# Kernel tuning notes

Measured on AMD Instinct MI355X. Metric: run time of the kernel, lower is better.

## Reference

```python
import jax, jax.numpy as jnp
import numpy as np
from jax.ops import segment_sum, segment_max

N_NODES = 16384
N_EDGES = 262144
NODE_DIM = 480
HIDDEN = 256
OUT_DIM = 128
HEADS = 4
N_GRAPHS = 256


def setup_inputs() -> dict:
    key = jax.random.key(0)
    ks = jax.random.split(key, 40)
    p = {}
    p['x'] = jax.random.normal(ks[0], (N_NODES, NODE_DIM), jnp.float32)
    p['edge_index'] = jax.random.randint(ks[1], (2, N_EDGES), 0, N_NODES)
    p['edge_attr'] = jax.random.uniform(ks[2], (N_EDGES, 1), dtype=jnp.float32)
    p['batch'] = jnp.sort(jax.random.randint(ks[3], (N_NODES,), 0, N_GRAPHS))
    p['num_graphs'] = N_GRAPHS
    def w(k, shape):
        return jax.random.normal(k, shape, jnp.float32) * 0.05
    i = 4
    for l, (din, h, c) in zip((1, 2, 3), [(NODE_DIM, HEADS, HIDDEN // HEADS), (HIDDEN, HEADS, HIDDEN // HEADS), (HIDDEN, 1, OUT_DIM)]):
        dout = h * c
        p[f'Wl{l}'] = w(ks[i], (din, dout)); i += 1
        p[f'bl{l}'] = jnp.zeros((dout,), jnp.float32)
        p[f'Wr{l}'] = w(ks[i], (din, dout)); i += 1
        p[f'br{l}'] = jnp.zeros((dout,), jnp.float32)
        p[f'We{l}'] = w(ks[i], (1, dout)); i += 1
        p[f'att{l}'] = w(ks[i], (h, c)); i += 1
        p[f'bo{l}'] = jnp.zeros((dout,), jnp.float32)
    for l, d in [(1, HIDDEN), (2, HIDDEN), (3, OUT_DIM)]:
        p[f'g{l}'] = jnp.ones((d,), jnp.float32)
        p[f'b{l}'] = jnp.zeros((d,), jnp.float32)
    p['Wres'] = w(ks[i], (NODE_DIM, HIDDEN))
    return p


def _layer_norm(x, g, b):
    mu = x.mean(-1, keepdims=True)
    v = ((x - mu) ** 2).mean(-1, keepdims=True)
    return (x - mu) * jax.lax.rsqrt(v + 1e-5) * g + b


def _gatv2(x, src, dst, ea, Wl, bl, Wr, br, We, att, bias):
    # PyG GATv2Conv, eval mode (dropout off), add_self_loops=True, fill_value='mean'
    N = x.shape[0]
    H, C = att.shape
    # self-loop edge attr = scatter-mean of incoming edge attrs per node
    deg = segment_sum(jnp.ones((src.shape[0],), x.dtype), dst, num_segments=N)
    loop_ea = segment_sum(ea, dst, num_segments=N) / jnp.maximum(deg, 1.0)[:, None]
    ar = jnp.arange(N, dtype=src.dtype)
    src2 = jnp.concatenate([src, ar])
    dst2 = jnp.concatenate([dst, ar])
    ea2 = jnp.concatenate([ea, loop_ea], axis=0)
    xl = (x @ Wl + bl).reshape(N, H, C)
    xr = (x @ Wr + br).reshape(N, H, C)
    e = (ea2 @ We).reshape(-1, H, C)
    m = jax.nn.leaky_relu(xl[src2] + xr[dst2] + e, 0.2)  # [E', H, C]
    alpha = jnp.einsum('ehc,hc->eh', m, att)
    amax = segment_max(alpha, dst2, num_segments=N)  # [N, H]; every node has a self loop
    ex = jnp.exp(alpha - amax[dst2])
    denom = segment_sum(ex, dst2, num_segments=N)
    a = ex / denom[dst2]
    out = segment_sum(a[:, :, None] * xl[src2], dst2, num_segments=N)  # [N, H, C]
    return out.reshape(N, H * C) + bias


def _forward(x, edge_attr, params, edge_index, batch, num_graphs):
    (Wl1, bl1, Wr1, br1, We1, att1, bo1,
     Wl2, bl2, Wr2, br2, We2, att2, bo2,
     Wl3, bl3, Wr3, br3, We3, att3, bo3,
     g1, b1, g2, b2, g3, b3, Wres) = params
    src, dst = edge_index[0], edge_index[1]
    gelu = lambda t: jax.nn.gelu(t, approximate=False)
    h = gelu(_layer_norm(_gatv2(x, src, dst, edge_attr, Wl1, bl1, Wr1, br1, We1, att1, bo1), g1, b1))
    h = h + x @ Wres
    h2 = gelu(_layer_norm(_gatv2(h, src, dst, edge_attr, Wl2, bl2, Wr2, br2, We2, att2, bo2), g2, b2))
    h2 = h2 + h
    h3 = _layer_norm(_gatv2(h2, src, dst, edge_attr, Wl3, bl3, Wr3, br3, We3, att3, bo3), g3, b3)
    # global mean pool over graphs
    sums = segment_sum(h3, batch, num_segments=num_graphs)
    cnt = segment_sum(jnp.ones((h3.shape[0],), h3.dtype), batch, num_segments=num_graphs)
    return sums / jnp.maximum(cnt, 1.0)[:, None]


def reference(x, edge_index, edge_attr, batch, num_graphs,
              Wl1, bl1, Wr1, br1, We1, att1, bo1,
              Wl2, bl2, Wr2, br2, We2, att2, bo2,
              Wl3, bl3, Wr3, br3, We3, att3, bo3,
              g1, b1, g2, b2, g3, b3, Wres):
    params = (Wl1, bl1, Wr1, br1, We1, att1, bo1,
              Wl2, bl2, Wr2, br2, We2, att2, bo2,
              Wl3, bl3, Wr3, br3, We3, att3, bo3,
              g1, b1, g2, b2, g3, b3, Wres)
    return _forward(x, edge_attr, params, edge_index, batch, num_graphs)
```

## Files before the change

### kernel.cpp

```cpp
#include <hip/hip_runtime.h>
#include <hip/hip_bf16.h>
#include <math.h>

#define NN 16384
#define NE 262144
#define KDIM1 480
#define DHID 256
#define DOUT3 128
#define NG 256

typedef short bf16x8 __attribute__((ext_vector_type(8)));
typedef float f32x4 __attribute__((ext_vector_type(4)));

#define LOG2E 1.44269504088896340736f

__device__ __forceinline__ unsigned short f2bf(float f) {
  unsigned u = __float_as_uint(f);
  unsigned r = (u + 0x7fffu + ((u >> 16) & 1u)) >> 16;
  return (unsigned short)r;
}
__device__ __forceinline__ float bf2f(unsigned short u) {
  return __uint_as_float((unsigned)u << 16);
}

__device__ __forceinline__ void gload_lds16(const void* g, void* l) {
  __builtin_amdgcn_global_load_lds((const __attribute__((address_space(1))) void*)g,
                                   (__attribute__((address_space(3))) void*)l,
                                   16, 0, 0);
}

__device__ __forceinline__ int lower_bound_i(const int* arr, int n, int val) {
  int lo = 0, hi = n;
  while (lo < hi) {
    int mid = (lo + hi) >> 1;
    if (arr[mid] < val) lo = mid + 1; else hi = mid;
  }
  return lo;
}


__global__ __launch_bounds__(256) void k_edge_count(const int* __restrict__ ei,
                                                    const float* __restrict__ ea,
                                                    int* __restrict__ deg,
                                                    float* __restrict__ easum) {
  int e = blockIdx.x * 256 + threadIdx.x;
  if (e >= NE) return;
  int d = ei[NE + e];
  atomicAdd(&deg[d], 1);
  atomicAdd(&easum[d], ea[e]);
}

__global__ __launch_bounds__(1024) void k_scan(const int* __restrict__ deg,
                                               float* __restrict__ easum,
                                               int* __restrict__ offs,
                                               int* __restrict__ cursor,
                                               const int* __restrict__ bat,
                                               float* __restrict__ ginv) {
  __shared__ int sums[1024];
  int t = threadIdx.x;
  int base = t * 16;
  int local[16];
  int s = 0;
#pragma unroll
  for (int i = 0; i < 16; ++i) { local[i] = deg[base + i]; s += local[i]; }
  sums[t] = s;
  __syncthreads();
  for (int d = 1; d < 1024; d <<= 1) {
    int v = (t >= d) ? sums[t - d] : 0;
    __syncthreads();
    sums[t] += v;
    __syncthreads();
  }
  int prefix = (t == 0) ? 0 : sums[t - 1];
#pragma unroll
  for (int i = 0; i < 16; ++i) {
    offs[base + i] = prefix;
    cursor[base + i] = prefix;
    prefix += local[i];
  }
  if (t == 1023) offs[NN] = prefix;
#pragma unroll
  for (int i = 0; i < 16; ++i) {
    easum[base + i] = easum[base + i] / fmaxf((float)local[i], 1.f);
  }
  if (t < NG) {
    int lo = lower_bound_i(bat, NN, t);
    int hi = lower_bound_i(bat, NN, t + 1);
    ginv[t] = 1.f / fmaxf((float)(hi - lo), 1.f);
  }
}

__global__ __launch_bounds__(256) void k_fill_csr(const int* __restrict__ ei,
                                                  const float* __restrict__ ea,
                                                  int* __restrict__ cursor,
                                                  int* __restrict__ csr_src,
                                                  float* __restrict__ csr_ea) {
  int e = blockIdx.x * 256 + threadIdx.x;
  if (e >= NE) return;
  int s = ei[e];
  int d = ei[NE + e];
  int pos = atomicAdd(&cursor[d], 1);
  csr_src[pos] = s;
  csr_ea[pos] = ea[e];
}


#define PREP_S0 (NN * KDIM1 / 4)
#define PREP_S1 (3 * DHID * KDIM1)
#define PREP_S2 (2 * DHID * DHID)
#define PREP_S3 (2 * DOUT3 * DHID)
#define PREP_TOTAL (PREP_S0 + PREP_S1 + PREP_S2 + PREP_S3)

__global__ __launch_bounds__(256) void k_prep(
    const float* __restrict__ x,
    const float* __restrict__ Wl1, const float* __restrict__ Wr1,
    const float* __restrict__ Wres,
    const float* __restrict__ Wl2, const float* __restrict__ Wr2,
    const float* __restrict__ Wl3, const float* __restrict__ Wr3,
    unsigned short* __restrict__ actb0, unsigned short* __restrict__ Wc1e,
    unsigned short* __restrict__ Wc2, unsigned short* __restrict__ Wc3) {
  int idx = blockIdx.x * 256 + threadIdx.x;
  if (idx < PREP_S0) {
    int i = idx * 4;
    float4 v = *(const float4*)&x[i];
    ushort4 o;
    o.x = f2bf(v.x); o.y = f2bf(v.y); o.z = f2bf(v.z); o.w = f2bf(v.w);
    *(ushort4*)&actb0[i] = o;
    return;
  }
  idx -= PREP_S0;
  if (idx < PREP_S1) {
    int n = idx / KDIM1, k = idx % KDIM1;
    float v;
    if (n < DHID)            v = Wl1[(size_t)k * DHID + n];
    else if (n < 2 * DHID)   v = Wr1[(size_t)k * DHID + (n - DHID)];
    else                     v = Wres[(size_t)k * DHID + (n - 2 * DHID)];
    Wc1e[idx] = f2bf(v);
    return;
  }
  idx -= PREP_S1;
  if (idx < PREP_S2) {
    int n = idx / DHID, k = idx % DHID;
    float v = (n < DHID) ? Wl2[(size_t)k * DHID + n] : Wr2[(size_t)k * DHID + (n - DHID)];
    Wc2[idx] = f2bf(v);
    return;
  }
  idx -= PREP_S2;
  if (idx < PREP_S3) {
    int n = idx / DHID, k = idx % DHID;
    float v = (n < DOUT3) ? Wl3[(size_t)k * DOUT3 + n] : Wr3[(size_t)k * DOUT3 + (n - DOUT3)];
    Wc3[idx] = f2bf(v);
  }
}


#define GEMM_CORE128(A_, Bt_, K_)                                                \
  __shared__ short As[128 * 32];                                                 \
  __shared__ short Bs[128 * 32];                                                 \
  int t = threadIdx.x;                                                           \
  int w = t >> 6;                                                                \
  int lane = t & 63;                                                             \
  int bm = blockIdx.y * 128;                                                     \
  int bn = blockIdx.x * 128;                                                     \
  int wr = w >> 1, wc = w & 1;                                                   \
  const short* Ag0 = A_ + (size_t)(bm + w * 16 + (lane >> 2)) * K_ + (lane & 3) * 8;        \
  const short* Ag1 = A_ + (size_t)(bm + 64 + w * 16 + (lane >> 2)) * K_ + (lane & 3) * 8;   \
  const short* Bg0 = Bt_ + (size_t)(bn + w * 16 + (lane >> 2)) * K_ + (lane & 3) * 8;       \
  const short* Bg1 = Bt_ + (size_t)(bn + 64 + w * 16 + (lane >> 2)) * K_ + (lane & 3) * 8;  \
  short* Al0 = &As[w * 16 * 32];                                                 \
  short* Al1 = &As[(64 + w * 16) * 32];                                          \
  short* Bl0 = &Bs[w * 16 * 32];                                                 \
  short* Bl1 = &Bs[(64 + w * 16) * 32];                                          \
  f32x4 acc[4][4] = {};                                                          \
  for (int k0 = 0; k0 < K_; k0 += 32) {                                          \
    gload_lds16(Ag0, Al0);                                                       \
    gload_lds16(Ag1, Al1);                                                       \
    gload_lds16(Bg0, Bl0);                                                       \
    gload_lds16(Bg1, Bl1);                                                       \
    Ag0 += 32; Ag1 += 32; Bg0 += 32; Bg1 += 32;                                  \
    __syncthreads();                                                             \
    bf16x8 af[4], bfv[4];                                                        \
    _Pragma("unroll")                                                            \
    for (int mi = 0; mi < 4; ++mi)                                               \
      af[mi] = *(const bf16x8*)&As[(wr * 64 + mi * 16 + (lane & 15)) * 32 + (lane >> 4) * 8]; \
    _Pragma("unroll")                                                            \
    for (int ni = 0; ni < 4; ++ni)                                               \
      bfv[ni] = *(const bf16x8*)&Bs[(wc * 64 + ni * 16 + (lane & 15)) * 32 + (lane >> 4) * 8]; \
    _Pragma("unroll")                                                            \
    for (int mi = 0; mi < 4; ++mi)                                               \
      _Pragma("unroll")                                                          \
      for (int ni = 0; ni < 4; ++ni)                                             \
        acc[mi][ni] = __builtin_amdgcn_mfma_f32_16x16x32_bf16(af[mi], bfv[ni], acc[mi][ni], 0, 0, 0); \
    __syncthreads();                                                             \
  }                                                                              \
  int col = lane & 15;                                                           \
  int row4 = (lane >> 4) * 4;

__global__ __launch_bounds__(256) void gemm_lrr(const short* __restrict__ A,
                                                const short* __restrict__ Wt,
                                                const float* __restrict__ bl,
                                                const float* __restrict__ br,
                                                unsigned short* __restrict__ xlb,
                                                unsigned short* __restrict__ xrb,
                                                float* __restrict__ xres,
                                                int K, int NH) {
  GEMM_CORE128(A, Wt, K)
  int seg = bn / NH;
  int cbase = bn - seg * NH;
#pragma unroll
  for (int mi = 0; mi < 4; ++mi) {
#pragma unroll
    for (int ni = 0; ni < 4; ++ni) {
      f32x4 a = acc[mi][ni];
      int gc = cbase + wc * 64 + ni * 16 + col;
      if (seg == 2) {
#pragma unroll
        for (int r = 0; r < 4; ++r) {
          int gr = bm + wr * 64 + mi * 16 + row4 + r;
          xres[(size_t)gr * NH + gc] = a[r];
        }
      } else {
        const float* bias = seg ? br : bl;
        unsigned short* outp = seg ? xrb : xlb;
        float bv = bias[gc];
#pragma unroll
        for (int r = 0; r < 4; ++r) {
          int gr = bm + wr * 64 + mi * 16 + row4 + r;
          outp[(size_t)gr * NH + gc] = f2bf(a[r] + bv);
        }
      }
    }
  }
}

__global__ __launch_bounds__(256) void gemm_lr(const short* __restrict__ A,
                                               const short* __restrict__ Wt,
                                               const float* __restrict__ bl,
                                               const float* __restrict__ br,
                                               unsigned short* __restrict__ xlb,
                                               unsigned short* __restrict__ xrb,
                                               int K, int NH) {
  GEMM_CORE128(A, Wt, K)
  bool right = (bn >= NH);
  unsigned short* outp = right ? xrb : xlb;
  const float* bias = right ? br : bl;
  int cbase = right ? bn - NH : bn;
#pragma unroll
  for (int mi = 0; mi < 4; ++mi) {
#pragma unroll
    for (int ni = 0; ni < 4; ++ni) {
      f32x4 a = acc[mi][ni];
      int gc = cbase + wc * 64 + ni * 16 + col;
      float bv = bias[gc];
#pragma unroll
      for (int r = 0; r < 4; ++r) {
        int gr = bm + wr * 64 + mi * 16 + row4 + r;
        outp[(size_t)gr * NH + gc] = f2bf(a[r] + bv);
      }
    }
  }
}


template<int D, int H, bool GELU_, bool RES_, bool WF32, bool WBF16, bool POOL>
__global__ __launch_bounds__(256) void gat_fused(
    const unsigned short* __restrict__ xlb, const unsigned short* __restrict__ xrb,
    const float* __restrict__ We, const float* __restrict__ att,
    const float* __restrict__ bo,
    const int* __restrict__ offs, const int* __restrict__ csr_src,
    const float* __restrict__ csr_ea, const float* __restrict__ loop_ea,
    const float* __restrict__ g, const float* __restrict__ bln,
    const float* __restrict__ res,
    float* __restrict__ outf, unsigned short* __restrict__ outb,
    const int* __restrict__ batch, const float* __restrict__ ginv,
    float* __restrict__ outp) {
  constexpr int P = D / 64;
  constexpr int C = D / H;
  constexpr int GROUP = C / P;
  int n = (blockIdx.x * blockDim.x + threadIdx.x) >> 6;
  int lane = threadIdx.x & 63;
  if (n >= NN) return;
  int d0 = lane * P;

  float wev[P], attv[P], xrv[P];
  if constexpr (P == 4) {
    *(float4*)wev = *(const float4*)&We[d0];
    *(float4*)attv = *(const float4*)&att[d0];
    ushort4 u = *(const ushort4*)&xrb[(size_t)n * D + d0];
    xrv[0] = bf2f(u.x); xrv[1] = bf2f(u.y); xrv[2] = bf2f(u.z); xrv[3] = bf2f(u.w);
  } else {
    *(float2*)wev = *(const float2*)&We[d0];
    *(float2*)attv = *(const float2*)&att[d0];
    ushort2 u = *(const ushort2*)&xrb[(size_t)n * D + d0];
    xrv[0] = bf2f(u.x); xrv[1] = bf2f(u.y);
  }
#pragma unroll
  for (int p = 0; p < P; ++p) attv[p] *= LOG2E;

#define GATHER(dst, srcidx)                                                  \
  {                                                                          \
    if constexpr (P == 4) {                                                  \
      ushort4 u_ = *(const ushort4*)&xlb[(size_t)(srcidx) * D + d0];         \
      dst[0] = bf2f(u_.x); dst[1] = bf2f(u_.y);                              \
      dst[2] = bf2f(u_.z); dst[3] = bf2f(u_.w);                              \
    } else {                                                                 \
      ushort2 u_ = *(const ushort2*)&xlb[(size_t)(srcidx) * D + d0];         \
      dst[0] = bf2f(u_.x); dst[1] = bf2f(u_.y);                              \
    }                                                                        \
  }

#define ALPHA(out_, xv_, eav_)                                               \
  {                                                                          \
    float partial_ = 0.f;                                                    \
    _Pragma("unroll")                                                        \
    for (int p = 0; p < P; ++p) {                                            \
      float s_ = xv_[p] + xrv[p] + (eav_) * wev[p];                          \
      s_ = fmaxf(s_, 0.2f * s_);                                             \
      partial_ = fmaf(s_, attv[p], partial_);                                \
    }                                                                        \
    _Pragma("unroll")                                                        \
    for (int w_ = 1; w_ < GROUP; w_ <<= 1) partial_ += __shfl_xor(partial_, w_, 64); \
    out_ = partial_;                                                         \
  }

  float acc[P];
  float xs[P];
  GATHER(xs, n)
  float m;
  ALPHA(m, xs, loop_ea[n])
  float l = 1.f;
#pragma unroll
  for (int p = 0; p < P; ++p) acc[p] = xs[p];

  int beg = offs[n];
  int cnt = offs[n + 1] - beg;
  int sbeg = __builtin_amdgcn_readfirstlane(beg);
  int scnt = __builtin_amdgcn_readfirstlane(cnt);

  int e = 0;
  for (; e + 4 <= scnt; e += 4) {
    int src0 = csr_src[sbeg + e];
    int src1 = csr_src[sbeg + e + 1];
    int src2 = csr_src[sbeg + e + 2];
    int src3 = csr_src[sbeg + e + 3];
    float ea0 = csr_ea[sbeg + e];
    float ea1 = csr_ea[sbeg + e + 1];
    float ea2 = csr_ea[sbeg + e + 2];
    float ea3 = csr_ea[sbeg + e + 3];
    float xv0[P], xv1[P], xv2[P], xv3[P];
    GATHER(xv0, src0)
    GATHER(xv1, src1)
    GATHER(xv2, src2)
    GATHER(xv3, src3)
    float a0, a1, a2, a3;
    ALPHA(a0, xv0, ea0)
    ALPHA(a1, xv1, ea1)
    ALPHA(a2, xv2, ea2)
    ALPHA(a3, xv3, ea3)
    float nm = fmaxf(fmaxf(m, fmaxf(a0, a1)), fmaxf(a2, a3));
    float sc = exp2f(m - nm);
    float pe0 = exp2f(a0 - nm);
    float pe1 = exp2f(a1 - nm);
    float pe2 = exp2f(a2 - nm);
    float pe3 = exp2f(a3 - nm);
    l = fmaf(l, sc, (pe0 + pe1) + (pe2 + pe3));
#pragma unroll
    for (int p = 0; p < P; ++p)
      acc[p] = fmaf(acc[p], sc,
                    fmaf(pe0, xv0[p], fmaf(pe1, xv1[p], fmaf(pe2, xv2[p], pe3 * xv3[p]))));
    m = nm;
  }
  for (; e < scnt; ++e) {
    int src0 = csr_src[sbeg + e];
    float ea0 = csr_ea[sbeg + e];
    float xv0[P];
    GATHER(xv0, src0)
    float a0;
    ALPHA(a0, xv0, ea0)
    float nm = fmaxf(m, a0);
    float sc = exp2f(m - nm);
    float pe0 = exp2f(a0 - nm);
    l = fmaf(l, sc, pe0);
#pragma unroll
    for (int p = 0; p < P; ++p) acc[p] = fmaf(acc[p], sc, pe0 * xv0[p]);
    m = nm;
  }
#undef GATHER
#undef ALPHA

  float inv = 1.f / l;
  float y[P];
#pragma unroll
  for (int p = 0; p < P; ++p) y[p] = fmaf(acc[p], inv, bo[d0 + p]);

  float s = 0.f, s2 = 0.f;
#pragma unroll
  for (int p = 0; p < P; ++p) { s += y[p]; s2 = fmaf(y[p], y[p], s2); }
#pragma unroll
  for (int w = 1; w < 64; w <<= 1) {
    s += __shfl_xor(s, w, 64);
    s2 += __shfl_xor(s2, w, 64);
  }
  float mu = s * (1.f / D);
  float var = s2 * (1.f / D) - mu * mu;
  float rr = rsqrtf(var + 1e-5f);

  float z[P];
#pragma unroll
  for (int p = 0; p < P; ++p) {
    float v = (y[p] - mu) * rr * g[d0 + p] + bln[d0 + p];
    if (GELU_) v = 0.5f * v * (1.f + erff(v * 0.70710678118654752f));
    if (RES_) v += res[(size_t)n * D + d0 + p];
    z[p] = v;
  }
  if (WF32) {
    float* orow = outf + (size_t)n * D;
    if constexpr (P == 4) *(float4*)&orow[d0] = *(float4*)z;
    else                  *(float2*)&orow[d0] = *(float2*)z;
  }
  if (WBF16) {
    unsigned short* orow = outb + (size_t)n * D;
    if constexpr (P == 4) {
      ushort4 o; o.x = f2bf(z[0]); o.y = f2bf(z[1]); o.z = f2bf(z[2]); o.w = f2bf(z[3]);
      *(ushort4*)&orow[d0] = o;
    } else {
      ushort2 o; o.x = f2bf(z[0]); o.y = f2bf(z[1]);
      *(ushort2*)&orow[d0] = o;
    }
  }
  if (POOL) {
    int gr = batch[n];
    float wgt = ginv[gr];
#pragma unroll
    for (int p = 0; p < P; ++p)
      atomicAdd(&outp[gr * D + d0 + p], z[p] * wgt);
  }
}


extern "C" void kernel_launch(void* const* d_in, const int* in_sizes, int n_in,
                              void* d_out, int out_size, void* d_ws, size_t ws_size,
                              hipStream_t stream) {
  const float* x   = (const float*)d_in[0];
  const int*   ei  = (const int*)d_in[1];
  const float* ea  = (const float*)d_in[2];
  const int*   bat = (const int*)d_in[3];
  const float* Wl1 = (const float*)d_in[5];  const float* bl1 = (const float*)d_in[6];
  const float* Wr1 = (const float*)d_in[7];  const float* br1 = (const float*)d_in[8];
  const float* We1 = (const float*)d_in[9];  const float* at1 = (const float*)d_in[10];
  const float* bo1 = (const float*)d_in[11];
  const float* Wl2 = (const float*)d_in[12]; const float* bl2 = (const float*)d_in[13];
  const float* Wr2 = (const float*)d_in[14]; const float* br2 = (const float*)d_in[15];
  const float* We2 = (const float*)d_in[16]; const float* at2 = (const float*)d_in[17];
  const float* bo2 = (const float*)d_in[18];
  const float* Wl3 = (const float*)d_in[19]; const float* bl3 = (const float*)d_in[20];
  const float* Wr3 = (const float*)d_in[21]; const float* br3 = (const float*)d_in[22];
  const float* We3 = (const float*)d_in[23]; const float* at3 = (const float*)d_in[24];
  const float* bo3 = (const float*)d_in[25];
  const float* g1 = (const float*)d_in[26]; const float* b1 = (const float*)d_in[27];
  const float* g2 = (const float*)d_in[28]; const float* b2 = (const float*)d_in[29];
  const float* g3 = (const float*)d_in[30]; const float* b3 = (const float*)d_in[31];
  const float* Wres = (const float*)d_in[32];
  float* out = (float*)d_out;

  char* ws = (char*)d_ws;
  size_t off = 0;
  int*   deg    = (int*)(ws + off); off += NN * 4;
  float* easum  = (float*)(ws + off); off += NN * 4;
  size_t zero_bytes = off;
  unsigned short* xlb = (unsigned short*)(ws + off); off += (size_t)NN * DHID * 2;
  unsigned short* xrb = (unsigned short*)(ws + off); off += (size_t)NN * DHID * 2;
  float* hb   = (float*)(ws + off); off += (size_t)NN * DHID * 4;
  float* xres = (float*)(ws + off); off += (size_t)NN * DHID * 4;
  unsigned short* actb0 = (unsigned short*)(ws + off); off += (size_t)NN * KDIM1 * 2;
  unsigned short* actb1 = (unsigned short*)(ws + off); off += (size_t)NN * DHID * 2;
  int*   offs   = (int*)(ws + off); off += (NN + 1) * 4 + 60;
  int*   cursor = (int*)(ws + off); off += NN * 4;
  float* ginv   = (float*)(ws + off); off += NG * 4;
  int*   csr_src = (int*)(ws + off); off += (size_t)NE * 4;
  float* csr_ea  = (float*)(ws + off); off += (size_t)NE * 4;
  unsigned short* Wc1e = (unsigned short*)(ws + off); off += (size_t)3 * DHID * KDIM1 * 2;
  unsigned short* Wc2  = (unsigned short*)(ws + off); off += (size_t)2 * DHID * DHID * 2;
  unsigned short* Wc3  = (unsigned short*)(ws + off); off += (size_t)2 * DOUT3 * DHID * 2;

  hipMemsetAsync(deg, 0, zero_bytes, stream);
  hipMemsetAsync(out, 0, (size_t)NG * DOUT3 * 4, stream);
  k_edge_count<<<NE / 256, 256, 0, stream>>>(ei, ea, deg, easum);
  k_scan<<<1, 1024, 0, stream>>>(deg, easum, offs, cursor, bat, ginv);
  k_fill_csr<<<NE / 256, 256, 0, stream>>>(ei, ea, cursor, csr_src, csr_ea);
  k_prep<<<(PREP_TOTAL + 255) / 256, 256, 0, stream>>>(x, Wl1, Wr1, Wres, Wl2, Wr2, Wl3, Wr3,
                                                       actb0, Wc1e, Wc2, Wc3);

  dim3 blk(256);
  int nwave_blocks = NN / 4;

  gemm_lrr<<<dim3(3 * DHID / 128, NN / 128), blk, 0, stream>>>(
      (const short*)actb0, (const short*)Wc1e, bl1, br1, xlb, xrb, xres, KDIM1, DHID);
  gat_fused<DHID, 4, true, true, true, true, false><<<nwave_blocks, blk, 0, stream>>>(
      xlb, xrb, We1, at1, bo1, offs, csr_src, csr_ea, easum, g1, b1, xres, hb, actb1,
      nullptr, nullptr, nullptr);

  gemm_lr<<<dim3(2 * DHID / 128, NN / 128), blk, 0, stream>>>(
      (const short*)actb1, (const short*)Wc2, bl2, br2, xlb, xrb, DHID, DHID);
  gat_fused<DHID, 4, true, true, false, true, false><<<nwave_blocks, blk, 0, stream>>>(
      xlb, xrb, We2, at2, bo2, offs, csr_src, csr_ea, easum, g2, b2, hb, nullptr, actb1,
      nullptr, nullptr, nullptr);

  gemm_lr<<<dim3(2 * DOUT3 / 128, NN / 128), blk, 0, stream>>>(
      (const short*)actb1, (const short*)Wc3, bl3, br3, xlb, xrb, DHID, DOUT3);
  gat_fused<DOUT3, 1, false, false, false, false, true><<<nwave_blocks, blk, 0, stream>>>(
      xlb, xrb, We3, at3, bo3, offs, csr_src, csr_ea, easum, g3, b3, nullptr, nullptr, nullptr,
      bat, ginv, out);
}
```

Before: 223.6 us.

## Split each node's edge list across two wavefronts and merge softmax state via LDS

The fused GAT aggregation kernel now assigns two wavefronts per destination node. Each processes half of the incoming edges with its own online-softmax state (max, sum, accumulator), and the first also handles the self-loop. The second wave writes its partial state to shared memory, and after a block barrier the first wave rescales and merges both before the bias, LayerNorm and epilogue. This doubles the number of waves to expose more memory-level parallelism for the gathers. In exchange it adds a barrier, an LDS round-trip, and waves that exit early and leave half the block idle during the epilogue.

```diff
diff --git a/kernel.cpp b/kernel.cpp
--- a/kernel.cpp
+++ b/kernel.cpp
@@ -277,9 +277,15 @@
   constexpr int P = D / 64;
   constexpr int C = D / H;
   constexpr int GROUP = C / P;
-  int n = (blockIdx.x * blockDim.x + threadIdx.x) >> 6;
+  __shared__ float lsm[4 * 64];
+  __shared__ float lsl[4 * 64];
+  __shared__ float lsacc[4 * 64 * P];
+
+  int wv = threadIdx.x >> 6;
   int lane = threadIdx.x & 63;
-  if (n >= NN) return;
+  int gw = blockIdx.x * 4 + wv;
+  int n = gw >> 1;
+  int sub = gw & 1;
   int d0 = lane * P;
 
   float wev[P], attv[P], xrv[P];
@@ -324,34 +330,43 @@
   }
 
   float acc[P];
-  float xs[P];
-  GATHER(xs, n)
-  float m;
-  ALPHA(m, xs, loop_ea[n])
-  float l = 1.f;
-#pragma unroll
-  for (int p = 0; p < P; ++p) acc[p] = xs[p];
-
+  float m, l;
   int beg = offs[n];
   int cnt = offs[n + 1] - beg;
   int sbeg = __builtin_amdgcn_readfirstlane(beg);
   int scnt = __builtin_amdgcn_readfirstlane(cnt);
-
-  int e = 0;
-  for (; e + 4 <= scnt; e += 4) {
-    int src0 = csr_src[sbeg + e];
-    int src1 = csr_src[sbeg + e + 1];
-    int src2 = csr_src[sbeg + e + 2];
-    int src3 = csr_src[sbeg + e + 3];
+  int h = scnt >> 1;
+
+  int e, eend;
+  if (sub == 0) {
+    float xs[P];
+    GATHER(xs, n)
+    ALPHA(m, xs, loop_ea[n])
+    l = 1.f;
+#pragma unroll
+    for (int p = 0; p < P; ++p) acc[p] = xs[p];
+    e = 0; eend = h;
+  } else {
+    m = -INFINITY; l = 0.f;
+#pragma unroll
+    for (int p = 0; p < P; ++p) acc[p] = 0.f;
+    e = h; eend = scnt;
+  }
+
+  for (; e + 4 <= eend; e += 4) {
+    int s0 = csr_src[sbeg + e];
+    int s1 = csr_src[sbeg + e + 1];
+    int s2 = csr_src[sbeg + e + 2];
+    int s3 = csr_src[sbeg + e + 3];
     float ea0 = csr_ea[sbeg + e];
     float ea1 = csr_ea[sbeg + e + 1];
     float ea2 = csr_ea[sbeg + e + 2];
     float ea3 = csr_ea[sbeg + e + 3];
     float xv0[P], xv1[P], xv2[P], xv3[P];
-    GATHER(xv0, src0)
-    GATHER(xv1, src1)
-    GATHER(xv2, src2)
-    GATHER(xv3, src3)
+    GATHER(xv0, s0)
+    GATHER(xv1, s1)
+    GATHER(xv2, s2)
+    GATHER(xv3, s3)
     float a0, a1, a2, a3;
     ALPHA(a0, xv0, ea0)
     ALPHA(a1, xv1, ea1)
@@ -370,11 +385,11 @@
                     fmaf(pe0, xv0[p], fmaf(pe1, xv1[p], fmaf(pe2, xv2[p], pe3 * xv3[p]))));
     m = nm;
   }
-  for (; e < scnt; ++e) {
-    int src0 = csr_src[sbeg + e];
+  for (; e < eend; ++e) {
+    int s0 = csr_src[sbeg + e];
     float ea0 = csr_ea[sbeg + e];
     float xv0[P];
-    GATHER(xv0, src0)
+    GATHER(xv0, s0)
     float a0;
     ALPHA(a0, xv0, ea0)
     float nm = fmaxf(m, a0);
@@ -387,6 +402,26 @@
   }
 #undef GATHER
 #undef ALPHA
+
+  if (sub == 1) {
+    int sl = wv * 64 + lane;
+    lsm[sl] = m; lsl[sl] = l;
+#pragma unroll
+    for (int p = 0; p < P; ++p) lsacc[sl * P + p] = acc[p];
+  }
+  __syncthreads();
+  if (sub == 1) return;
+  {
+    int ps = (wv + 1) * 64 + lane;
+    float m1 = lsm[ps], l1 = lsl[ps];
+    float nm = fmaxf(m, m1);
+    float s0 = exp2f(m - nm);
+    float s1 = exp2f(m1 - nm);
+    l = l * s0 + l1 * s1;
+#pragma unroll
+    for (int p = 0; p < P; ++p) acc[p] = acc[p] * s0 + lsacc[ps * P + p] * s1;
+    m = nm;
+  }
 
   float inv = 1.f / l;
   float y[P];
@@ -492,23 +527,23 @@
                                                        actb0, Wc1e, Wc2, Wc3);
 
   dim3 blk(256);
-  int nwave_blocks = NN / 4;
+  int gat_blocks = NN / 2;
 
   gemm_lrr<<<dim3(3 * DHID / 128, NN / 128), blk, 0, stream>>>(
       (const short*)actb0, (const short*)Wc1e, bl1, br1, xlb, xrb, xres, KDIM1, DHID);
-  gat_fused<DHID, 4, true, true, true, true, false><<<nwave_blocks, blk, 0, stream>>>(
+  gat_fused<DHID, 4, true, true, true, true, false><<<gat_blocks, blk, 0, stream>>>(
       xlb, xrb, We1, at1, bo1, offs, csr_src, csr_ea, easum, g1, b1, xres, hb, actb1,
       nullptr, nullptr, nullptr);
 
   gemm_lr<<<dim3(2 * DHID / 128, NN / 128), blk, 0, stream>>>(
       (const short*)actb1, (const short*)Wc2, bl2, br2, xlb, xrb, DHID, DHID);
-  gat_fused<DHID, 4, true, true, false, true, false><<<nwave_blocks, blk, 0, stream>>>(
+  gat_fused<DHID, 4, true, true, false, true, false><<<gat_blocks, blk, 0, stream>>>(
       xlb, xrb, We2, at2, bo2, offs, csr_src, csr_ea, easum, g2, b2, hb, nullptr, actb1,
       nullptr, nullptr, nullptr);
 
   gemm_lr<<<dim3(2 * DOUT3 / 128, NN / 128), blk, 0, stream>>>(
       (const short*)actb1, (const short*)Wc3, bl3, br3, xlb, xrb, DHID, DOUT3);
-  gat_fused<DOUT3, 1, false, false, false, false, true><<<nwave_blocks, blk, 0, stream>>>(
+  gat_fused<DOUT3, 1, false, false, false, false, true><<<gat_blocks, blk, 0, stream>>>(
       xlb, xrb, We3, at3, bo3, offs, csr_src, csr_ea, easum, g3, b3, nullptr, nullptr, nullptr,
       bat, ginv, out);
 }
```

Result: slower. 262.0 us (+17.2%).
